# Optimization experiments

Measured on AMD Instinct MI355X. Metric: run time of the kernel, lower is better.

The kernel has to match this reference:

```python
import jax, jax.numpy as jnp
import numpy as np

N, L, C = 32, 2048, 128
DEM = 8


def setup_inputs() -> dict:
    key = jax.random.key(0)
    ks = jax.random.split(key, 8)
    return {
        "inp0": jax.random.normal(ks[0], (N, L, C), jnp.float32),
        "inp1": jax.random.normal(ks[1], (N, L, C), jnp.float32),
        "inp2": jax.random.normal(ks[2], (N, L, C), jnp.float32),
        "dem": jax.random.normal(ks[3], (N, DEM), jnp.float32),
        "W1": jax.random.normal(ks[4], (DEM, 40), jnp.float32) * (1.0 / np.sqrt(DEM)),
        "b1": jnp.zeros((40,), jnp.float32),
        "W2": jax.random.normal(ks[5], (40, 20), jnp.float32) * (1.0 / np.sqrt(40.0)),
        "b2": jnp.zeros((20,), jnp.float32),
    }


def _causal_pools(x):
    # x: [N, L, C]. Left zero-padding of (L-1) + kernel-L pool at stride 1
    # == causal prefix pools (padding zeros participate in max/avg windows).
    Lt = x.shape[1]
    t = jnp.arange(Lt)
    cmax = jax.lax.cummax(x, axis=1)                       # prefix max of real values
    has_pad = (t < Lt - 1)[None, :, None]                  # windows that still contain pad zeros
    p_max = jnp.where(has_pad, jnp.maximum(cmax, 0.0), cmax)

    def combine(a, b):
        av, ai = a
        bv, bi = b
        take_b = bv > av
        return jnp.where(take_b, bv, av), jnp.where(take_b, bi, ai)

    idx0 = jnp.broadcast_to(t[None, :, None], x.shape).astype(jnp.int32)
    _, amax = jax.lax.associative_scan(combine, (x, idx0), axis=1)
    # if a pad zero is the window max, torch's index (shifted by L-1) points to a
    # (negative) pad position: first pad slot of window t maps to t-(L-1)
    pad_idx = (t - (Lt - 1))[None, :, None].astype(jnp.int32)
    p_max_ind = jnp.where(has_pad & (cmax < 0.0), pad_idx, amax)

    csum = jnp.cumsum(x, axis=1)
    p_avg = csum / jnp.asarray(Lt, x.dtype)               # avg_pool1d counts pad zeros -> /L
    cnt = (t + 1).astype(x.dtype)[None, :, None]
    p_sum = csum / cnt                                     # norm_sum: sum normalized by #real steps
    return p_max, p_max_ind, p_avg, p_sum


def reference(inp0, inp1, inp2, dem, W1, b1, W2, b2):
    patient = []
    inds = []
    acts = []
    for x in (inp0, inp1, inp2):
        p_max, p_max_ind, p_avg, p_sum = _causal_pools(x)
        patient.append(jnp.concatenate([p_max, p_avg, p_sum], axis=-1))
        inds.append(p_max_ind)
        acts.append(jax.lax.stop_gradient(p_max))
    d = jax.nn.relu(jax.nn.relu(dem @ W1 + b1) @ W2 + b2)   # [N, 20]
    d = jnp.broadcast_to(d[:, None, :], (d.shape[0], L, d.shape[-1]))
    out = jnp.concatenate(patient + [d], axis=-1)           # [N, L, 3*384 + 20]
    return (out, inds[0], inds[1], inds[2], acts[0], acts[1], acts[2])
```

## Files before the change

### kernel.cpp

```cpp
#include <hip/hip_runtime.h>
#include <float.h>

#define Nn 32
#define Ll 2048
#define Cc 128
#define NTILES 64
#define TILE 32
#define OUTC 1172
#define NLC (Nn * Ll * Cc)
#define OUT_ELEMS ((size_t)Nn * Ll * OUTC)
#define NUNITS (3 * Nn * NTILES)
#define AGG (NUNITS * Cc)

typedef float  f4 __attribute__((ext_vector_type(4)));
typedef int    i4 __attribute__((ext_vector_type(4)));

__device__ __forceinline__ void nts4(f4* p, f4 v) { __builtin_nontemporal_store(v, p); }
__device__ __forceinline__ void nts1(float* p, float v) { __builtin_nontemporal_store(v, p); }

__global__ __launch_bounds__(256) void k_agg(
        const float* __restrict__ x0, const float* __restrict__ x1,
        const float* __restrict__ x2,
        f4* __restrict__ aggMax, i4* __restrict__ aggIdx, f4* __restrict__ aggSum) {
    int unit = blockIdx.x * 8 + (threadIdx.x >> 5);
    int lane = threadIdx.x & 31;
    int inp = unit >> 11;
    int rem = unit & 2047;
    int n = rem >> 6;
    int tile = rem & 63;
    const float* x = (inp == 0) ? x0 : ((inp == 1) ? x1 : x2);
    int t0 = tile * TILE;
    const f4* p = (const f4*)(x + ((size_t)n * Ll + t0) * Cc) + lane;

    f4 m = { -FLT_MAX, -FLT_MAX, -FLT_MAX, -FLT_MAX };
    i4 mi = { 0, 0, 0, 0 };
    f4 s = { 0.f, 0.f, 0.f, 0.f };
#pragma unroll 4
    for (int tl = 0; tl < TILE; ++tl) {
        f4 v = p[(size_t)tl * (Cc / 4)];
        int t = t0 + tl;
#pragma unroll
        for (int j = 0; j < 4; ++j) {
            s[j] += v[j];
            if (v[j] > m[j]) { m[j] = v[j]; mi[j] = t; }
        }
    }
    int o = unit * (Cc / 4) + lane;
    aggMax[o] = m; aggIdx[o] = mi; aggSum[o] = s;
}

__global__ __launch_bounds__(256) void k_scan_mlp(
        float* __restrict__ aggMax, int* __restrict__ aggIdx, float* __restrict__ aggSum,
        const float* __restrict__ dem, const float* __restrict__ W1,
        const float* __restrict__ b1, const float* __restrict__ W2,
        const float* __restrict__ b2, float* __restrict__ dvals) {
    if (blockIdx.x < 48) {
        int tid = blockIdx.x * 256 + threadIdx.x;
        int inp = tid / (Nn * Cc);
        int rem = tid - inp * (Nn * Cc);
        int n = rem >> 7;
        int c = rem & 127;
        int base = ((inp * Nn + n) * NTILES) * Cc + c;

        float m = -FLT_MAX; int mi = 0; float s = 0.f;
#pragma unroll 4
        for (int j = 0; j < NTILES; ++j) {
            int o = base + j * Cc;
            float am = aggMax[o]; int ai = aggIdx[o]; float as = aggSum[o];
            aggMax[o] = m; aggIdx[o] = mi; aggSum[o] = s;
            if (am > m) { m = am; mi = ai; }
            s += as;
        }
    } else {
        int n = threadIdx.x;
        if (n >= Nn) return;
        float h[40];
        float de[8];
#pragma unroll
        for (int k = 0; k < 8; ++k) de[k] = dem[n * 8 + k];
#pragma unroll
        for (int j = 0; j < 40; ++j) {
            float s = b1[j];
#pragma unroll
            for (int k = 0; k < 8; ++k) s += de[k] * W1[k * 40 + j];
            h[j] = fmaxf(s, 0.f);
        }
#pragma unroll
        for (int o = 0; o < 20; ++o) {
            float s = b2[o];
#pragma unroll
            for (int j = 0; j < 40; ++j) s += h[j] * W2[j * 20 + o];
            dvals[n * 20 + o] = fmaxf(s, 0.f);
        }
    }
}

__global__ __launch_bounds__(256) void k_apply(
        const float* __restrict__ x0, const float* __restrict__ x1,
        const float* __restrict__ x2,
        const f4* __restrict__ aggMax, const i4* __restrict__ aggIdx,
        const f4* __restrict__ aggSum, const float* __restrict__ dvals,
        float* __restrict__ out) {
    int unit = blockIdx.x * 8 + (threadIdx.x >> 5);
    int lane = threadIdx.x & 31;
    int inp = unit >> 11;
    int rem = unit & 2047;
    int n = rem >> 6;
    int tile = rem & 63;
    const float* x = (inp == 0) ? x0 : ((inp == 1) ? x1 : x2);
    int t0 = tile * TILE;

    int o = unit * (Cc / 4) + lane;
    f4 m = aggMax[o]; i4 mi = aggIdx[o]; f4 s = aggSum[o];

    float dv = 0.f;
    if (inp == 0 && lane < 20) dv = dvals[n * 20 + lane];

    const f4* p = (const f4*)(x + ((size_t)n * Ll + t0) * Cc) + lane;
    f4* omax = (f4*)(out + (size_t)n * Ll * OUTC + (size_t)t0 * OUTC + inp * 384) + lane;
    f4* oind = (f4*)(out + OUT_ELEMS + (size_t)inp * NLC + ((size_t)n * Ll + t0) * Cc) + lane;
    f4* oact = (f4*)(out + OUT_ELEMS + 3 * (size_t)NLC + (size_t)inp * NLC + ((size_t)n * Ll + t0) * Cc) + lane;
    float* dout = out + (size_t)n * Ll * OUTC + (size_t)t0 * OUTC + 1152 + (lane < 20 ? lane : 0);

    const float invL = 1.0f / (float)Ll;
#pragma unroll 4
    for (int tl = 0; tl < TILE; ++tl) {
        f4 v = p[(size_t)tl * (Cc / 4)];
        int t = t0 + tl;
        bool haspad = (t < Ll - 1);
        float rcnt = __builtin_amdgcn_rcpf((float)(t + 1));
        f4 pmax, pidx, pavg, psum;
#pragma unroll
        for (int j = 0; j < 4; ++j) {
            s[j] += v[j];
            if (v[j] > m[j]) { m[j] = v[j]; mi[j] = t; }
            float cmax = m[j];
            pmax[j] = haspad ? fmaxf(cmax, 0.f) : cmax;
            pidx[j] = (float)((haspad && cmax < 0.f) ? (t - (Ll - 1)) : mi[j]);
            pavg[j] = s[j] * invL;
            psum[j] = s[j] * rcnt;
        }
        size_t ro = (size_t)tl * (OUTC / 4);
        nts4(&omax[ro],          pmax);
        nts4(&omax[ro + Cc / 4], pavg);
        nts4(&omax[ro + Cc / 2], psum);
        nts4(&oind[(size_t)tl * (Cc / 4)], pidx);
        nts4(&oact[(size_t)tl * (Cc / 4)], pmax);
        if (inp == 0 && lane < 20)
            nts1(&dout[(size_t)tl * OUTC], dv);
    }
}

extern "C" void kernel_launch(void* const* d_in, const int* in_sizes, int n_in,
                              void* d_out, int out_size, void* d_ws, size_t ws_size,
                              hipStream_t stream) {
    const float* x0  = (const float*)d_in[0];
    const float* x1  = (const float*)d_in[1];
    const float* x2  = (const float*)d_in[2];
    const float* dem = (const float*)d_in[3];
    const float* W1  = (const float*)d_in[4];
    const float* b1  = (const float*)d_in[5];
    const float* W2  = (const float*)d_in[6];
    const float* b2  = (const float*)d_in[7];
    float* out = (float*)d_out;

    char* ws = (char*)d_ws;
    float* aggMax = (float*)ws;
    int*   aggIdx = (int*)(ws + (size_t)AGG * 4);
    float* aggSum = (float*)(ws + 2 * (size_t)AGG * 4);
    float* dvals  = (float*)(ws + 3 * (size_t)AGG * 4);

    k_agg<<<dim3(NUNITS / 8), dim3(256), 0, stream>>>(x0, x1, x2,
        (f4*)aggMax, (i4*)aggIdx, (f4*)aggSum);
    k_scan_mlp<<<dim3(49), dim3(256), 0, stream>>>(aggMax, aggIdx, aggSum,
        dem, W1, b1, W2, b2, dvals);
    k_apply<<<dim3(NUNITS / 8), dim3(256), 0, stream>>>(x0, x1, x2,
        (const f4*)aggMax, (const i4*)aggIdx, (const f4*)aggSum, dvals, out);
}
```

Measured before the change: 648.4 us.

## Drop separate scan kernel; compute tile prefix inside apply, fold MLP into agg

```diff
diff --git a/kernel.cpp b/kernel.cpp
--- a/kernel.cpp
+++ b/kernel.cpp
@@ -4,8 +4,8 @@
 #define Nn 32
 #define Ll 2048
 #define Cc 128
-#define NTILES 64
-#define TILE 32
+#define NTILES 32
+#define TILE 64
 #define OUTC 1172
 #define NLC (Nn * Ll * Cc)
 #define OUT_ELEMS ((size_t)Nn * Ll * OUTC)
@@ -21,61 +21,14 @@
 __global__ __launch_bounds__(256) void k_agg(
         const float* __restrict__ x0, const float* __restrict__ x1,
         const float* __restrict__ x2,
-        f4* __restrict__ aggMax, i4* __restrict__ aggIdx, f4* __restrict__ aggSum) {
-    int unit = blockIdx.x * 8 + (threadIdx.x >> 5);
-    int lane = threadIdx.x & 31;
-    int inp = unit >> 11;
-    int rem = unit & 2047;
-    int n = rem >> 6;
-    int tile = rem & 63;
-    const float* x = (inp == 0) ? x0 : ((inp == 1) ? x1 : x2);
-    int t0 = tile * TILE;
-    const f4* p = (const f4*)(x + ((size_t)n * Ll + t0) * Cc) + lane;
-
-    f4 m = { -FLT_MAX, -FLT_MAX, -FLT_MAX, -FLT_MAX };
-    i4 mi = { 0, 0, 0, 0 };
-    f4 s = { 0.f, 0.f, 0.f, 0.f };
-#pragma unroll 4
-    for (int tl = 0; tl < TILE; ++tl) {
-        f4 v = p[(size_t)tl * (Cc / 4)];
-        int t = t0 + tl;
-#pragma unroll
-        for (int j = 0; j < 4; ++j) {
-            s[j] += v[j];
-            if (v[j] > m[j]) { m[j] = v[j]; mi[j] = t; }
-        }
-    }
-    int o = unit * (Cc / 4) + lane;
-    aggMax[o] = m; aggIdx[o] = mi; aggSum[o] = s;
-}
-
-__global__ __launch_bounds__(256) void k_scan_mlp(
-        float* __restrict__ aggMax, int* __restrict__ aggIdx, float* __restrict__ aggSum,
+        f4* __restrict__ aggMax, i4* __restrict__ aggIdx, f4* __restrict__ aggSum,
         const float* __restrict__ dem, const float* __restrict__ W1,
         const float* __restrict__ b1, const float* __restrict__ W2,
         const float* __restrict__ b2, float* __restrict__ dvals) {
-    if (blockIdx.x < 48) {
-        int tid = blockIdx.x * 256 + threadIdx.x;
-        int inp = tid / (Nn * Cc);
-        int rem = tid - inp * (Nn * Cc);
-        int n = rem >> 7;
-        int c = rem & 127;
-        int base = ((inp * Nn + n) * NTILES) * Cc + c;
-
-        float m = -FLT_MAX; int mi = 0; float s = 0.f;
-#pragma unroll 4
-        for (int j = 0; j < NTILES; ++j) {
-            int o = base + j * Cc;
-            float am = aggMax[o]; int ai = aggIdx[o]; float as = aggSum[o];
-            aggMax[o] = m; aggIdx[o] = mi; aggSum[o] = s;
-            if (am > m) { m = am; mi = ai; }
-            s += as;
-        }
-    } else {
+    if (blockIdx.x == NUNITS / 8) {
         int n = threadIdx.x;
         if (n >= Nn) return;
-        float h[40];
-        float de[8];
+        float de[8], h[40];
 #pragma unroll
         for (int k = 0; k < 8; ++k) de[k] = dem[n * 8 + k];
 #pragma unroll
@@ -92,7 +45,34 @@
             for (int j = 0; j < 40; ++j) s += h[j] * W2[j * 20 + o];
             dvals[n * 20 + o] = fmaxf(s, 0.f);
         }
+        return;
     }
+
+    int unit = blockIdx.x * 8 + (threadIdx.x >> 5);
+    int lane = threadIdx.x & 31;
+    int inp = unit >> 10;
+    int rem = unit & 1023;
+    int n = rem >> 5;
+    int tile = rem & 31;
+    const float* x = (inp == 0) ? x0 : ((inp == 1) ? x1 : x2);
+    int t0 = tile * TILE;
+    const f4* p = (const f4*)(x + ((size_t)n * Ll + t0) * Cc) + lane;
+
+    f4 m = { -FLT_MAX, -FLT_MAX, -FLT_MAX, -FLT_MAX };
+    i4 mi = { 0, 0, 0, 0 };
+    f4 s = { 0.f, 0.f, 0.f, 0.f };
+#pragma unroll 8
+    for (int tl = 0; tl < TILE; ++tl) {
+        f4 v = p[(size_t)tl * (Cc / 4)];
+        int t = t0 + tl;
+#pragma unroll
+        for (int j = 0; j < 4; ++j) {
+            s[j] += v[j];
+            if (v[j] > m[j]) { m[j] = v[j]; mi[j] = t; }
+        }
+    }
+    int o = unit * (Cc / 4) + lane;
+    aggMax[o] = m; aggIdx[o] = mi; aggSum[o] = s;
 }
 
 __global__ __launch_bounds__(256) void k_apply(
@@ -103,15 +83,27 @@
         float* __restrict__ out) {
     int unit = blockIdx.x * 8 + (threadIdx.x >> 5);
     int lane = threadIdx.x & 31;
-    int inp = unit >> 11;
-    int rem = unit & 2047;
-    int n = rem >> 6;
-    int tile = rem & 63;
+    int inp = unit >> 10;
+    int rem = unit & 1023;
+    int n = rem >> 5;
+    int tile = rem & 31;
     const float* x = (inp == 0) ? x0 : ((inp == 1) ? x1 : x2);
     int t0 = tile * TILE;
 
-    int o = unit * (Cc / 4) + lane;
-    f4 m = aggMax[o]; i4 mi = aggIdx[o]; f4 s = aggSum[o];
+    f4 m = { -FLT_MAX, -FLT_MAX, -FLT_MAX, -FLT_MAX };
+    i4 mi = { 0, 0, 0, 0 };
+    f4 s = { 0.f, 0.f, 0.f, 0.f };
+    int rowbase = (unit - tile) * (Cc / 4) + lane;
+#pragma unroll 4
+    for (int j = 0; j < tile; ++j) {
+        int o = rowbase + j * (Cc / 4);
+        f4 am = aggMax[o]; i4 ai = aggIdx[o]; f4 as = aggSum[o];
+#pragma unroll
+        for (int jj = 0; jj < 4; ++jj) {
+            if (am[jj] > m[jj]) { m[jj] = am[jj]; mi[jj] = ai[jj]; }
+            s[jj] += as[jj];
+        }
+    }
 
     float dv = 0.f;
     if (inp == 0 && lane < 20) dv = dvals[n * 20 + lane];
@@ -170,10 +162,8 @@
     float* aggSum = (float*)(ws + 2 * (size_t)AGG * 4);
     float* dvals  = (float*)(ws + 3 * (size_t)AGG * 4);
 
-    k_agg<<<dim3(NUNITS / 8), dim3(256), 0, stream>>>(x0, x1, x2,
-        (f4*)aggMax, (i4*)aggIdx, (f4*)aggSum);
-    k_scan_mlp<<<dim3(49), dim3(256), 0, stream>>>(aggMax, aggIdx, aggSum,
-        dem, W1, b1, W2, b2, dvals);
+    k_agg<<<dim3(NUNITS / 8 + 1), dim3(256), 0, stream>>>(x0, x1, x2,
+        (f4*)aggMax, (i4*)aggIdx, (f4*)aggSum, dem, W1, b1, W2, b2, dvals);
     k_apply<<<dim3(NUNITS / 8), dim3(256), 0, stream>>>(x0, x1, x2,
         (const f4*)aggMax, (const i4*)aggIdx, (const f4*)aggSum, dvals, out);
 }
```

Result: faster. 618.7 us (-4.6%).
